# Kernel tuning notes

Measured on AMD Instinct MI355X. Metric: run time of the kernel, lower is better.

## Reference

```python
import jax, jax.numpy as jnp
import numpy as np

N_NODES = 50000
N_EDGES = 800000
N_REL = 16
N_GRAPHS = 64
IN_DIM = 128
HID = 128
FC = 256
N_CLASSES = 16


def setup_inputs() -> dict:
    key = jax.random.key(0)
    ks = jax.random.split(key, 16)
    h = jax.random.normal(ks[0], (N_NODES, IN_DIM), dtype=jnp.float32)
    src = jax.random.randint(ks[1], (N_EDGES,), 0, N_NODES, dtype=jnp.int32)
    dst = jax.random.randint(ks[2], (N_EDGES,), 0, N_NODES, dtype=jnp.int32)
    rel_types = jax.random.randint(ks[3], (N_EDGES,), 0, N_REL, dtype=jnp.int32)
    graph_ids = jnp.sort(jax.random.randint(ks[4], (N_NODES,), 0, N_GRAPHS, dtype=jnp.int32))
    s1 = 1.0 / np.sqrt(IN_DIM)
    s2 = 1.0 / np.sqrt(HID)
    # RGCN layer 1: per-relation weights, self-loop weight, bias
    W1 = jax.random.normal(ks[5], (N_REL, IN_DIM, HID), dtype=jnp.float32) * s1
    Ws1 = jax.random.normal(ks[6], (IN_DIM, HID), dtype=jnp.float32) * s1
    b1 = jnp.zeros((HID,), dtype=jnp.float32)
    # RGCN layer 2
    W2 = jax.random.normal(ks[7], (N_REL, HID, HID), dtype=jnp.float32) * s2
    Ws2 = jax.random.normal(ks[8], (HID, HID), dtype=jnp.float32) * s2
    b2 = jnp.zeros((HID,), dtype=jnp.float32)
    # FC layer after mean pooling
    Wfc = jax.random.normal(ks[9], (HID, FC), dtype=jnp.float32) * s2
    bfc = jnp.zeros((FC,), dtype=jnp.float32)
    # classify head
    Wc = jax.random.normal(ks[10], (FC, N_CLASSES), dtype=jnp.float32) * (1.0 / np.sqrt(FC))
    bc = jnp.zeros((N_CLASSES,), dtype=jnp.float32)
    return dict(h=h, src=src, dst=dst, rel_types=rel_types, graph_ids=graph_ids,
                W1=W1, Ws1=Ws1, b1=b1, W2=W2, Ws2=Ws2, b2=b2,
                Wfc=Wfc, bfc=bfc, Wc=Wc, bc=bc)


def _rel_graph_conv(h, W, Ws, b, src, dst, rel):
    # dgl RelGraphConv (regularizer=None, self_loop=True, bias=True):
    # out[v] = sum_{e:(u->v)} W[rel_e] @ h[u] + Ws @ h[v] + b
    hW = jnp.einsum('ni,rio->rno', h, W)            # [R, N, out]
    msg = hW[rel, src]                               # [E, out] gather per edge
    agg = jax.ops.segment_sum(msg, dst, num_segments=N_NODES)
    return agg + h @ Ws + b


def _mean_nodes(h, graph_ids):
    sums = jax.ops.segment_sum(h, graph_ids, num_segments=N_GRAPHS)      # [G, D]
    cnts = jax.ops.segment_sum(jnp.ones((h.shape[0], 1), h.dtype), graph_ids,
                               num_segments=N_GRAPHS)                    # [G, 1]
    return sums / jnp.maximum(cnts, 1.0)


def reference(h, src, dst, rel_types, graph_ids,
              W1, Ws1, b1, W2, Ws2, b2, Wfc, bfc, Wc, bc):
    h = h.astype(jnp.float32)
    h = jax.nn.relu(_rel_graph_conv(h, W1, Ws1, b1, src, dst, rel_types))
    h = jax.nn.relu(_rel_graph_conv(h, W2, Ws2, b2, src, dst, rel_types))
    hg = _mean_nodes(h, graph_ids)                   # [G, HID]
    hg = jax.nn.relu(hg @ Wfc + bfc)                 # [G, FC]
    return jax.nn.softmax(hg @ Wc + bc, axis=1)      # [G, n_classes]
```

## Files before the change

### kernel.cpp

```cpp
#include <hip/hip_runtime.h>
#include <hip/hip_bf16.h>

#define N_NODES   50000
#define N_PAD     50048
#define N_EDGES   800000
#define N_REL     16
#define N_GRAPHS  64
#define DIM       128
#define FC_DIM    256
#define N_CLASSES 16

#define NCOARSE   782
#define NCH       196
#define CHSZ      4096
#define POOL_CH   64

#define NBLK_CX   27200
#define XW_TOTAL  (N_PAD * DIM + 2 * 17 * 16384)

#define WS_HG     0
#define WS_CNT    32768
#define MEMSET_SZ 33024
#define WS_BLKH   33024
#define WS_COFS   646400
#define WS_RTMP   649728
#define WS_RECS   3849728
#define WS_OFFSDR 7049728
#define WS_X1     10253056
#define WS_X2     23065344
#define WS_AGG    35877632
#define WS_WB     48689920

typedef __attribute__((ext_vector_type(8))) short bf16x8;
typedef __attribute__((ext_vector_type(4))) float f32x4;

__device__ __forceinline__ void atomAddF(float* p, float v) {
#if defined(__gfx90a__) || defined(__gfx942__) || defined(__gfx950__)
    unsafeAtomicAdd(p, v);
#else
    atomicAdd(p, v);
#endif
}

__device__ __forceinline__ float bf2f(unsigned int u) {
    union { float f; unsigned int i; } x; x.i = u << 16; return x.f;
}
__device__ __forceinline__ unsigned short f2bf(float f) {
    union { float f; unsigned int u; } x; x.f = f;
    unsigned int r = x.u + 0x7fff + ((x.u >> 16) & 1);
    return (unsigned short)(r >> 16);
}
__device__ __forceinline__ void accum8(float* qa, uint4 u) {
    qa[0] += bf2f(u.x & 0xffff); qa[1] += bf2f(u.x >> 16);
    qa[2] += bf2f(u.y & 0xffff); qa[3] += bf2f(u.y >> 16);
    qa[4] += bf2f(u.z & 0xffff); qa[5] += bf2f(u.z >> 16);
    qa[6] += bf2f(u.w & 0xffff); qa[7] += bf2f(u.w >> 16);
}
__device__ __forceinline__ void pack16(const float* qa, unsigned short* dst) {
    #pragma unroll
    for (int j = 0; j < 2; ++j) {
        uint4 w;
        w.x = ((unsigned int)f2bf(qa[j*8+1]) << 16) | f2bf(qa[j*8+0]);
        w.y = ((unsigned int)f2bf(qa[j*8+3]) << 16) | f2bf(qa[j*8+2]);
        w.z = ((unsigned int)f2bf(qa[j*8+5]) << 16) | f2bf(qa[j*8+4]);
        w.w = ((unsigned int)f2bf(qa[j*8+7]) << 16) | f2bf(qa[j*8+6]);
        ((uint4*)dst)[j] = w;
    }
}

__global__ __launch_bounds__(256) void k_h1cx(
    const int* __restrict__ dst,
    int* __restrict__ blockHist,
    const float* __restrict__ h, unsigned short* __restrict__ x1,
    const float* __restrict__ W1, const float* __restrict__ Ws1,
    const float* __restrict__ W2, const float* __restrict__ Ws2,
    unsigned short* __restrict__ Wb)
{
    __shared__ int hl[NCOARSE];
    int t = threadIdx.x;
    if (blockIdx.x < NCH) {
        int b = blockIdx.x;
        for (int i = t; i < NCOARSE; i += 256) hl[i] = 0;
        __syncthreads();
        int e0 = b * CHSZ;
        int eend = min(e0 + CHSZ, N_EDGES);
        for (int e = e0 + t; e < eend; e += 256)
            atomicAdd(&hl[dst[e] >> 6], 1);
        __syncthreads();
        for (int i = t; i < NCOARSE; i += 256) blockHist[b * NCOARSE + i] = hl[i];
    } else {
        int id = (blockIdx.x - NCH) * 256 + t;
        if (id < N_PAD * DIM) {
            int v = id >> 7;
            x1[id] = (v < N_NODES) ? f2bf(h[id]) : (unsigned short)0;
        } else {
            int tt = id - N_PAD * DIM;
            int l = tt / 278528, rem = tt % 278528;
            int r = rem >> 14, rr = rem & 16383;
            int n = rr >> 7, k = rr & 127;
            const float* W  = l ? W2 : W1;
            const float* Ws = l ? Ws2 : Ws1;
            float v = (r < 16) ? W[r * 16384 + k * 128 + n] : Ws[k * 128 + n];
            Wb[tt] = f2bf(v);
        }
    }
}

__global__ __launch_bounds__(256) void k_csA(int* __restrict__ blockHist,
                                             int* __restrict__ cOffs)
{
    __shared__ int sc[2][256];
    int i = blockIdx.x, t = threadIdx.x;
    int v = (t < NCH) ? blockHist[t * NCOARSE + i] : 0;
    sc[0][t] = v; __syncthreads();
    int cur = 0;
    for (int o = 1; o < 256; o <<= 1) {
        sc[cur ^ 1][t] = sc[cur][t] + ((t >= o) ? sc[cur][t - o] : 0);
        __syncthreads();
        cur ^= 1;
    }
    if (t < NCH) blockHist[t * NCOARSE + i] = sc[cur][t] - v;
    if (t == NCH - 1) cOffs[i] = sc[cur][t];
}

__global__ __launch_bounds__(1024) void k_csB(int* __restrict__ cOffs)
{
    __shared__ int c1[1024], c2[1024];
    int t = threadIdx.x;
    int v = (t < NCOARSE) ? cOffs[t] : 0;
    c1[t] = v; __syncthreads();
    int* cur = c1; int* nxt = c2;
    for (int o = 1; o < 1024; o <<= 1) {
        nxt[t] = cur[t] + ((t >= o) ? cur[t - o] : 0);
        __syncthreads();
        int* tmp = cur; cur = nxt; nxt = tmp;
    }
    if (t < NCOARSE) cOffs[t] = cur[t] - v;
    if (t == NCOARSE) cOffs[NCOARSE] = cur[NCOARSE - 1];
}

__global__ __launch_bounds__(256) void k_scat1(
    const int* __restrict__ src, const int* __restrict__ dst, const int* __restrict__ rel,
    const int* __restrict__ blockHist, const int* __restrict__ cOffs,
    unsigned int* __restrict__ rtmp)
{
    __shared__ int baseL[NCOARSE];
    __shared__ int hl[NCOARSE];
    int b = blockIdx.x, t = threadIdx.x;
    for (int i = t; i < NCOARSE; i += 256) {
        baseL[i] = blockHist[b * NCOARSE + i] + cOffs[i];
        hl[i] = 0;
    }
    __syncthreads();
    int e0 = b * CHSZ;
    int eend = min(e0 + CHSZ, N_EDGES);
    for (int e = e0 + t; e < eend; e += 256) {
        int d = dst[e];
        int c = d >> 6;
        int rank = atomicAdd(&hl[c], 1);
        rtmp[baseL[c] + rank] = ((unsigned int)src[e] << 10)
                              | ((unsigned int)(d & 63) << 4)
                              | (unsigned int)rel[e];
    }
}

__global__ __launch_bounds__(256) void k_p2(
    const unsigned int* __restrict__ rtmp, const int* __restrict__ cOffs,
    unsigned int* __restrict__ recs, int* __restrict__ offsDR)
{
    __shared__ int cnt[1024];
    __shared__ int part[256], part2[256];
    int i = blockIdx.x, t = threadIdx.x;
    int segB = cOffs[i], segE = cOffs[i + 1];
    for (int k = t; k < 1024; k += 256) cnt[k] = 0;
    __syncthreads();
    for (int e = segB + t; e < segE; e += 256)
        atomicAdd(&cnt[rtmp[e] & 1023u], 1);
    __syncthreads();
    int b4 = t * 4;
    int s0 = cnt[b4], s1 = cnt[b4+1], s2 = cnt[b4+2], s3 = cnt[b4+3];
    int tsum = s0 + s1 + s2 + s3;
    part[t] = tsum;
    __syncthreads();
    int* cur = part; int* nxt = part2;
    for (int o = 1; o < 256; o <<= 1) {
        nxt[t] = cur[t] + ((t >= o) ? cur[t - o] : 0);
        __syncthreads();
        int* tmp = cur; cur = nxt; nxt = tmp;
    }
    int excl = cur[t] - tsum + segB;
    cnt[b4]     = excl;
    cnt[b4 + 1] = excl + s0;
    cnt[b4 + 2] = excl + s0 + s1;
    cnt[b4 + 3] = excl + s0 + s1 + s2;
    __syncthreads();
    for (int k = t; k < 1024; k += 256) offsDR[i * 1024 + k] = cnt[k];
    if (i == NCOARSE - 1 && t == 0) offsDR[NCOARSE * 1024] = segE;
    for (int e = segB + t; e < segE; e += 256) {
        unsigned int r = rtmp[e];
        int pos = atomicAdd(&cnt[r & 1023u], 1);
        recs[pos] = r >> 10;
    }
}

__global__ __launch_bounds__(256) void k_rgcn(
    const unsigned short* __restrict__ x, const unsigned short* __restrict__ Wb,
    const unsigned int* __restrict__ recs, const int* __restrict__ offsDR,
    const float* __restrict__ bias, unsigned short* __restrict__ out, int relu)
{
    __shared__ __attribute__((aligned(16))) unsigned short S[64 * 136];
    __shared__ int sOffs[1025];
    int tid = threadIdx.x;
    int bin = blockIdx.x;
    int v0 = bin * 64;
    for (int k = tid; k < 1025; k += 256) sOffs[k] = offsDR[bin * 1024 + k];

    int w = tid >> 6, l = tid & 63, nl = l & 15, q = l >> 4;
    int gh = tid >> 3, s = tid & 7;

    f32x4 acc[4][2];
    #pragma unroll
    for (int m = 0; m < 4; ++m) {
        acc[m][0] = (f32x4){0.f, 0.f, 0.f, 0.f};
        acc[m][1] = (f32x4){0.f, 0.f, 0.f, 0.f};
    }
    __syncthreads();

    for (int r = 0; r < 17; ++r) {
        #pragma unroll
        for (int hf = 0; hf < 2; ++hf) {
            int g = hf * 32 + gh;
            float qa[16];
            #pragma unroll
            for (int j = 0; j < 16; ++j) qa[j] = 0.f;
            if (r == 16) {
                const uint4* xp = (const uint4*)(x + (size_t)(v0 + g) * DIM + s * 16);
                uint4 u0 = xp[0], u1 = xp[1];
                accum8(qa, u0); accum8(qa + 8, u1);
            } else {
                int o0 = sOffs[g * 16 + r], o1 = sOffs[g * 16 + r + 1];
                for (int e = o0; e < o1; ++e) {
                    const uint4* xp = (const uint4*)(x + (size_t)recs[e] * DIM + s * 16);
                    uint4 u0 = xp[0], u1 = xp[1];
                    accum8(qa, u0); accum8(qa + 8, u1);
                }
            }
            pack16(qa, &S[g * 136 + s * 16]);
        }
        __syncthreads();
        const unsigned short* wr = Wb + r * 16384;
        #pragma unroll
        for (int kc = 0; kc < 4; ++kc) {
            bf16x8 b0 = *(const bf16x8*)(wr + (w * 32 + nl) * 128 + kc * 32 + q * 8);
            bf16x8 b1 = *(const bf16x8*)(wr + (w * 32 + 16 + nl) * 128 + kc * 32 + q * 8);
            #pragma unroll
            for (int m = 0; m < 4; ++m) {
                bf16x8 a = *(const bf16x8*)(&S[(m * 16 + nl) * 136 + kc * 32 + q * 8]);
                acc[m][0] = __builtin_amdgcn_mfma_f32_16x16x32_bf16(a, b0, acc[m][0], 0, 0, 0);
                acc[m][1] = __builtin_amdgcn_mfma_f32_16x16x32_bf16(a, b1, acc[m][1], 0, 0, 0);
            }
        }
        __syncthreads();
    }

    float bv0 = bias[w * 32 + nl], bv1 = bias[w * 32 + 16 + nl];
    #pragma unroll
    for (int m = 0; m < 4; ++m) {
        #pragma unroll
        for (int reg = 0; reg < 4; ++reg) {
            int row = m * 16 + q * 4 + reg;
            float f0 = acc[m][0][reg] + bv0;
            float f1 = acc[m][1][reg] + bv1;
            if (relu) { f0 = fmaxf(f0, 0.f); f1 = fmaxf(f1, 0.f); }
            S[row * 136 + (w * 32 + nl)]      = f2bf(f0);
            S[row * 136 + (w * 32 + 16 + nl)] = f2bf(f1);
        }
    }
    __syncthreads();
    {
        unsigned short* Ob = out + (size_t)v0 * DIM;
        #pragma unroll
        for (int it = 0; it < 4; ++it) {
            int c = tid + it * 256;
            int rw = c >> 4, k8 = c & 15;
            uint4 vv = *(const uint4*)(&S[rw * 136 + k8 * 8]);
            *(uint4*)(Ob + rw * DIM + k8 * 8) = vv;
        }
    }
}

__global__ void k_pool(const unsigned short* __restrict__ agg2, const int* __restrict__ gids,
                       float* __restrict__ hg_sum, int* __restrict__ cnt)
{
    int d  = threadIdx.x;
    int n0 = blockIdx.x * POOL_CH;
    int nend = min(n0 + POOL_CH, N_NODES);
    if (n0 >= N_NODES) return;
    int curg = gids[n0];
    float run = 0.f;
    for (int n = n0; n < nend; ++n) {
        int g = gids[n];
        if (g != curg) { atomAddF(&hg_sum[curg*DIM + d], run); run = 0.f; curg = g; }
        run += fmaxf(bf2f((unsigned int)agg2[n*DIM + d]), 0.f);
    }
    atomAddF(&hg_sum[curg*DIM + d], run);
    if (d == 0) {
        int cg = gids[n0]; int rl = 0;
        for (int n = n0; n < nend; ++n) {
            int g = gids[n];
            if (g != cg) { atomicAdd(&cnt[cg], rl); rl = 0; cg = g; }
            rl++;
        }
        atomicAdd(&cnt[cg], rl);
    }
}

__global__ __launch_bounds__(256) void k_head(
    const float* __restrict__ hg_sum, const int* __restrict__ cnt,
    const float* __restrict__ Wfc, const float* __restrict__ bfc,
    const float* __restrict__ Wc, const float* __restrict__ bc,
    float* __restrict__ out)
{
    int g = blockIdx.x, t = threadIdx.x;
    __shared__ float hgl[DIM];
    __shared__ float fcl[FC_DIM];
    __shared__ float lg[N_CLASSES];
    if (t < DIM) {
        float c = (float)max(cnt[g], 1);
        hgl[t] = hg_sum[g*DIM + t] / c;
    }
    __syncthreads();
    {
        float sv = bfc[t];
        #pragma unroll 4
        for (int k = 0; k < DIM; ++k) sv += hgl[k] * Wfc[k*FC_DIM + t];
        fcl[t] = fmaxf(sv, 0.f);
    }
    __syncthreads();
    if (t < N_CLASSES) {
        float lgt = bc[t];
        #pragma unroll 4
        for (int k = 0; k < FC_DIM; ++k) lgt += fcl[k] * Wc[k*N_CLASSES + t];
        lg[t] = lgt;
    }
    __syncthreads();
    if (t < N_CLASSES) {
        float m = lg[0];
        #pragma unroll
        for (int c = 1; c < N_CLASSES; ++c) m = fmaxf(m, lg[c]);
        float sden = 0.f;
        #pragma unroll
        for (int c = 0; c < N_CLASSES; ++c) sden += expf(lg[c] - m);
        out[g*N_CLASSES + t] = expf(lg[t] - m) / sden;
    }
}

extern "C" void kernel_launch(void* const* d_in, const int* in_sizes, int n_in,
                              void* d_out, int out_size, void* d_ws, size_t ws_size,
                              hipStream_t stream)
{
    const float* h   = (const float*)d_in[0];
    const int*   src = (const int*)d_in[1];
    const int*   dst = (const int*)d_in[2];
    const int*   rel = (const int*)d_in[3];
    const int*   gid = (const int*)d_in[4];
    const float* W1  = (const float*)d_in[5];
    const float* Ws1 = (const float*)d_in[6];
    const float* b1  = (const float*)d_in[7];
    const float* W2  = (const float*)d_in[8];
    const float* Ws2 = (const float*)d_in[9];
    const float* b2  = (const float*)d_in[10];
    const float* Wfc = (const float*)d_in[11];
    const float* bfc = (const float*)d_in[12];
    const float* Wc  = (const float*)d_in[13];
    const float* bc  = (const float*)d_in[14];
    float* out = (float*)d_out;

    char* ws = (char*)d_ws;
    float* hgsum = (float*)(ws + WS_HG);
    int*   cnt   = (int*)(ws + WS_CNT);
    int*   blkH  = (int*)(ws + WS_BLKH);
    int*   cOffs = (int*)(ws + WS_COFS);
    unsigned int* rtmp = (unsigned int*)(ws + WS_RTMP);
    unsigned int* recs = (unsigned int*)(ws + WS_RECS);
    int*   offsDR = (int*)(ws + WS_OFFSDR);
    unsigned short* x1  = (unsigned short*)(ws + WS_X1);
    unsigned short* x2  = (unsigned short*)(ws + WS_X2);
    unsigned short* agg = (unsigned short*)(ws + WS_AGG);
    unsigned short* Wb  = (unsigned short*)(ws + WS_WB);

    hipMemsetAsync(ws + WS_HG, 0, MEMSET_SZ, stream);

    k_h1cx<<<NCH + NBLK_CX, 256, 0, stream>>>(dst, blkH, h, x1, W1, Ws1, W2, Ws2, Wb);
    k_csA<<<NCOARSE, 256, 0, stream>>>(blkH, cOffs);
    k_csB<<<1, 1024, 0, stream>>>(cOffs);
    k_scat1<<<NCH, 256, 0, stream>>>(src, dst, rel, blkH, cOffs, rtmp);
    k_p2<<<NCOARSE, 256, 0, stream>>>(rtmp, cOffs, recs, offsDR);

    k_rgcn<<<NCOARSE, 256, 0, stream>>>(x1, Wb, recs, offsDR, b1, x2, 1);
    k_rgcn<<<NCOARSE, 256, 0, stream>>>(x2, Wb + 17 * 16384, recs, offsDR, b2, agg, 0);

    k_pool<<<(N_PAD + POOL_CH - 1) / POOL_CH, 128, 0, stream>>>(agg, gid, hgsum, cnt);
    k_head<<<N_GRAPHS, 256, 0, stream>>>(hgsum, cnt, Wfc, bfc, Wc, bc, out);
}
```

Before: 449.0 us.

## Halve RGCN node bins to 32 nodes and unroll edge gathers by four

Shrinks the coarse destination bin from 64 to 32 nodes, which doubles the number of RGCN blocks (1564) and halves each block's shared memory and accumulator registers. The scan, scatter and sort kernels are updated to match the new bin count and record encoding. The per-relation gather loop is unrolled by four so each thread has several independent row loads in flight. The cost is reloading the relation weights from memory in twice as many blocks, and each block issues half as many MFMAs per weight fetch.

```diff
diff --git a/kernel.cpp b/kernel.cpp
--- a/kernel.cpp
+++ b/kernel.cpp
@@ -10,7 +10,7 @@
 #define FC_DIM    256
 #define N_CLASSES 16
 
-#define NCOARSE   782
+#define NCOARSE   1564
 #define NCH       196
 #define CHSZ      4096
 #define POOL_CH   64
@@ -22,14 +22,14 @@
 #define WS_CNT    32768
 #define MEMSET_SZ 33024
 #define WS_BLKH   33024
-#define WS_COFS   646400
-#define WS_RTMP   649728
-#define WS_RECS   3849728
-#define WS_OFFSDR 7049728
-#define WS_X1     10253056
-#define WS_X2     23065344
-#define WS_AGG    35877632
-#define WS_WB     48689920
+#define WS_COFS   1259520
+#define WS_RTMP   1265920
+#define WS_RECS   4465920
+#define WS_OFFSDR 7665920
+#define WS_X1     10869248
+#define WS_X2     23681536
+#define WS_AGG    36493824
+#define WS_WB     49306112
 
 typedef __attribute__((ext_vector_type(8))) short bf16x8;
 typedef __attribute__((ext_vector_type(4))) float f32x4;
@@ -85,7 +85,7 @@
         int e0 = b * CHSZ;
         int eend = min(e0 + CHSZ, N_EDGES);
         for (int e = e0 + t; e < eend; e += 256)
-            atomicAdd(&hl[dst[e] >> 6], 1);
+            atomicAdd(&hl[dst[e] >> 5], 1);
         __syncthreads();
         for (int i = t; i < NCOARSE; i += 256) blockHist[b * NCOARSE + i] = hl[i];
     } else {
@@ -127,16 +127,21 @@
 {
     __shared__ int c1[1024], c2[1024];
     int t = threadIdx.x;
-    int v = (t < NCOARSE) ? cOffs[t] : 0;
-    c1[t] = v; __syncthreads();
+    int i0 = 2 * t, i1 = 2 * t + 1;
+    int v0 = (i0 < NCOARSE) ? cOffs[i0] : 0;
+    int v1 = (i1 < NCOARSE) ? cOffs[i1] : 0;
+    int p = v0 + v1;
+    c1[t] = p; __syncthreads();
     int* cur = c1; int* nxt = c2;
     for (int o = 1; o < 1024; o <<= 1) {
         nxt[t] = cur[t] + ((t >= o) ? cur[t - o] : 0);
         __syncthreads();
         int* tmp = cur; cur = nxt; nxt = tmp;
     }
-    if (t < NCOARSE) cOffs[t] = cur[t] - v;
-    if (t == NCOARSE) cOffs[NCOARSE] = cur[NCOARSE - 1];
+    int ex = cur[t] - p;
+    if (i0 < NCOARSE) cOffs[i0] = ex;
+    if (i1 < NCOARSE) cOffs[i1] = ex + v0;
+    if (t == 1023) cOffs[NCOARSE] = cur[1023];
 }
 
 __global__ __launch_bounds__(256) void k_scat1(
@@ -156,10 +161,10 @@
     int eend = min(e0 + CHSZ, N_EDGES);
     for (int e = e0 + t; e < eend; e += 256) {
         int d = dst[e];
-        int c = d >> 6;
+        int c = d >> 5;
         int rank = atomicAdd(&hl[c], 1);
-        rtmp[baseL[c] + rank] = ((unsigned int)src[e] << 10)
-                              | ((unsigned int)(d & 63) << 4)
+        rtmp[baseL[c] + rank] = ((unsigned int)src[e] << 9)
+                              | ((unsigned int)(d & 31) << 4)
                               | (unsigned int)rel[e];
     }
 }
@@ -168,18 +173,17 @@
     const unsigned int* __restrict__ rtmp, const int* __restrict__ cOffs,
     unsigned int* __restrict__ recs, int* __restrict__ offsDR)
 {
-    __shared__ int cnt[1024];
+    __shared__ int cnt[512];
     __shared__ int part[256], part2[256];
     int i = blockIdx.x, t = threadIdx.x;
     int segB = cOffs[i], segE = cOffs[i + 1];
-    for (int k = t; k < 1024; k += 256) cnt[k] = 0;
+    cnt[t] = 0; cnt[t + 256] = 0;
     __syncthreads();
     for (int e = segB + t; e < segE; e += 256)
-        atomicAdd(&cnt[rtmp[e] & 1023u], 1);
-    __syncthreads();
-    int b4 = t * 4;
-    int s0 = cnt[b4], s1 = cnt[b4+1], s2 = cnt[b4+2], s3 = cnt[b4+3];
-    int tsum = s0 + s1 + s2 + s3;
+        atomicAdd(&cnt[rtmp[e] & 511u], 1);
+    __syncthreads();
+    int s0 = cnt[2 * t], s1 = cnt[2 * t + 1];
+    int tsum = s0 + s1;
     part[t] = tsum;
     __syncthreads();
     int* cur = part; int* nxt = part2;
@@ -189,17 +193,16 @@
         int* tmp = cur; cur = nxt; nxt = tmp;
     }
     int excl = cur[t] - tsum + segB;
-    cnt[b4]     = excl;
-    cnt[b4 + 1] = excl + s0;
-    cnt[b4 + 2] = excl + s0 + s1;
-    cnt[b4 + 3] = excl + s0 + s1 + s2;
-    __syncthreads();
-    for (int k = t; k < 1024; k += 256) offsDR[i * 1024 + k] = cnt[k];
-    if (i == NCOARSE - 1 && t == 0) offsDR[NCOARSE * 1024] = segE;
+    cnt[2 * t]     = excl;
+    cnt[2 * t + 1] = excl + s0;
+    offsDR[i * 512 + 2 * t]     = excl;
+    offsDR[i * 512 + 2 * t + 1] = excl + s0;
+    if (i == NCOARSE - 1 && t == 0) offsDR[NCOARSE * 512] = segE;
+    __syncthreads();
     for (int e = segB + t; e < segE; e += 256) {
         unsigned int r = rtmp[e];
-        int pos = atomicAdd(&cnt[r & 1023u], 1);
-        recs[pos] = r >> 10;
+        int pos = atomicAdd(&cnt[r & 511u], 1);
+        recs[pos] = r >> 9;
     }
 }
 
@@ -208,45 +211,55 @@
     const unsigned int* __restrict__ recs, const int* __restrict__ offsDR,
     const float* __restrict__ bias, unsigned short* __restrict__ out, int relu)
 {
-    __shared__ __attribute__((aligned(16))) unsigned short S[64 * 136];
-    __shared__ int sOffs[1025];
+    __shared__ __attribute__((aligned(16))) unsigned short S[32 * 136];
+    __shared__ int sOffs[513];
     int tid = threadIdx.x;
     int bin = blockIdx.x;
-    int v0 = bin * 64;
-    for (int k = tid; k < 1025; k += 256) sOffs[k] = offsDR[bin * 1024 + k];
+    int v0 = bin * 32;
+    for (int k = tid; k < 513; k += 256) sOffs[k] = offsDR[bin * 512 + k];
 
     int w = tid >> 6, l = tid & 63, nl = l & 15, q = l >> 4;
-    int gh = tid >> 3, s = tid & 7;
-
-    f32x4 acc[4][2];
+    int g = tid >> 3, s = tid & 7;
+
+    f32x4 acc[2][2];
     #pragma unroll
-    for (int m = 0; m < 4; ++m) {
+    for (int m = 0; m < 2; ++m) {
         acc[m][0] = (f32x4){0.f, 0.f, 0.f, 0.f};
         acc[m][1] = (f32x4){0.f, 0.f, 0.f, 0.f};
     }
     __syncthreads();
 
     for (int r = 0; r < 17; ++r) {
-        #pragma unroll
-        for (int hf = 0; hf < 2; ++hf) {
-            int g = hf * 32 + gh;
-            float qa[16];
-            #pragma unroll
-            for (int j = 0; j < 16; ++j) qa[j] = 0.f;
-            if (r == 16) {
-                const uint4* xp = (const uint4*)(x + (size_t)(v0 + g) * DIM + s * 16);
+        float qa[16];
+        #pragma unroll
+        for (int j = 0; j < 16; ++j) qa[j] = 0.f;
+        if (r == 16) {
+            const uint4* xp = (const uint4*)(x + (size_t)(v0 + g) * DIM + s * 16);
+            uint4 u0 = xp[0], u1 = xp[1];
+            accum8(qa, u0); accum8(qa + 8, u1);
+        } else {
+            int o0 = sOffs[g * 16 + r], o1 = sOffs[g * 16 + r + 1];
+            int e = o0;
+            for (; e + 3 < o1; e += 4) {
+                unsigned int c0 = recs[e], c1 = recs[e+1], c2 = recs[e+2], c3 = recs[e+3];
+                const uint4* p0 = (const uint4*)(x + (size_t)c0 * DIM + s * 16);
+                const uint4* p1 = (const uint4*)(x + (size_t)c1 * DIM + s * 16);
+                const uint4* p2 = (const uint4*)(x + (size_t)c2 * DIM + s * 16);
+                const uint4* p3 = (const uint4*)(x + (size_t)c3 * DIM + s * 16);
+                uint4 a0 = p0[0], a1 = p0[1], b0 = p1[0], b1 = p1[1];
+                uint4 e0v = p2[0], e1v = p2[1], f0v = p3[0], f1v = p3[1];
+                accum8(qa, a0);  accum8(qa + 8, a1);
+                accum8(qa, b0);  accum8(qa + 8, b1);
+                accum8(qa, e0v); accum8(qa + 8, e1v);
+                accum8(qa, f0v); accum8(qa + 8, f1v);
+            }
+            for (; e < o1; ++e) {
+                const uint4* xp = (const uint4*)(x + (size_t)recs[e] * DIM + s * 16);
                 uint4 u0 = xp[0], u1 = xp[1];
                 accum8(qa, u0); accum8(qa + 8, u1);
-            } else {
-                int o0 = sOffs[g * 16 + r], o1 = sOffs[g * 16 + r + 1];
-                for (int e = o0; e < o1; ++e) {
-                    const uint4* xp = (const uint4*)(x + (size_t)recs[e] * DIM + s * 16);
-                    uint4 u0 = xp[0], u1 = xp[1];
-                    accum8(qa, u0); accum8(qa + 8, u1);
-                }
             }
-            pack16(qa, &S[g * 136 + s * 16]);
-        }
+        }
+        pack16(qa, &S[g * 136 + s * 16]);
         __syncthreads();
         const unsigned short* wr = Wb + r * 16384;
         #pragma unroll
@@ -254,7 +267,7 @@
             bf16x8 b0 = *(const bf16x8*)(wr + (w * 32 + nl) * 128 + kc * 32 + q * 8);
             bf16x8 b1 = *(const bf16x8*)(wr + (w * 32 + 16 + nl) * 128 + kc * 32 + q * 8);
             #pragma unroll
-            for (int m = 0; m < 4; ++m) {
+            for (int m = 0; m < 2; ++m) {
                 bf16x8 a = *(const bf16x8*)(&S[(m * 16 + nl) * 136 + kc * 32 + q * 8]);
                 acc[m][0] = __builtin_amdgcn_mfma_f32_16x16x32_bf16(a, b0, acc[m][0], 0, 0, 0);
                 acc[m][1] = __builtin_amdgcn_mfma_f32_16x16x32_bf16(a, b1, acc[m][1], 0, 0, 0);
@@ -265,7 +278,7 @@
 
     float bv0 = bias[w * 32 + nl], bv1 = bias[w * 32 + 16 + nl];
     #pragma unroll
-    for (int m = 0; m < 4; ++m) {
+    for (int m = 0; m < 2; ++m) {
         #pragma unroll
         for (int reg = 0; reg < 4; ++reg) {
             int row = m * 16 + q * 4 + reg;
@@ -280,7 +293,7 @@
     {
         unsigned short* Ob = out + (size_t)v0 * DIM;
         #pragma unroll
-        for (int it = 0; it < 4; ++it) {
+        for (int it = 0; it < 2; ++it) {
             int c = tid + it * 256;
             int rw = c >> 4, k8 = c & 15;
             uint4 vv = *(const uint4*)(&S[rw * 136 + k8 * 8]);
```

Result: slower. 536.4 us (+19.5%).

## Sort edges relation-major per bin and gather via shared-memory float atomics

Applied to the files above, without the earlier changes.

Records within each 64-node bin are now sorted relation-major instead of destination-major, so each relation's edges form one contiguous range. All 32 edge groups then process those edges in parallel, accumulating into a shared fp32 tile with LDS atomics. The next relation's gather overlaps with the current relation's MFMA, and the self-loop term loads the node rows directly. This removes the load imbalance of one thread group walking a single destination's edges, at the cost of many LDS atomic adds and a larger shared-memory footprint (about 34KB for accL) that may lower occupancy.

```diff
diff --git a/kernel.cpp b/kernel.cpp
--- a/kernel.cpp
+++ b/kernel.cpp
@@ -56,16 +56,11 @@
     qa[4] += bf2f(u.z & 0xffff); qa[5] += bf2f(u.z >> 16);
     qa[6] += bf2f(u.w & 0xffff); qa[7] += bf2f(u.w >> 16);
 }
-__device__ __forceinline__ void pack16(const float* qa, unsigned short* dst) {
-    #pragma unroll
-    for (int j = 0; j < 2; ++j) {
-        uint4 w;
-        w.x = ((unsigned int)f2bf(qa[j*8+1]) << 16) | f2bf(qa[j*8+0]);
-        w.y = ((unsigned int)f2bf(qa[j*8+3]) << 16) | f2bf(qa[j*8+2]);
-        w.z = ((unsigned int)f2bf(qa[j*8+5]) << 16) | f2bf(qa[j*8+4]);
-        w.w = ((unsigned int)f2bf(qa[j*8+7]) << 16) | f2bf(qa[j*8+6]);
-        ((uint4*)dst)[j] = w;
-    }
+__device__ __forceinline__ void atomAcc8(float* ar, uint4 u) {
+    atomicAdd(&ar[0], bf2f(u.x & 0xffff)); atomicAdd(&ar[1], bf2f(u.x >> 16));
+    atomicAdd(&ar[2], bf2f(u.y & 0xffff)); atomicAdd(&ar[3], bf2f(u.y >> 16));
+    atomicAdd(&ar[4], bf2f(u.z & 0xffff)); atomicAdd(&ar[5], bf2f(u.z >> 16));
+    atomicAdd(&ar[6], bf2f(u.w & 0xffff)); atomicAdd(&ar[7], bf2f(u.w >> 16));
 }
 
 __global__ __launch_bounds__(256) void k_h1cx(
@@ -159,8 +154,8 @@
         int c = d >> 6;
         int rank = atomicAdd(&hl[c], 1);
         rtmp[baseL[c] + rank] = ((unsigned int)src[e] << 10)
-                              | ((unsigned int)(d & 63) << 4)
-                              | (unsigned int)rel[e];
+                              | ((unsigned int)rel[e] << 6)
+                              | (unsigned int)(d & 63);
     }
 }
 
@@ -189,17 +184,20 @@
         int* tmp = cur; cur = nxt; nxt = tmp;
     }
     int excl = cur[t] - tsum + segB;
+    offsDR[i * 1024 + b4]     = excl;
+    offsDR[i * 1024 + b4 + 1] = excl + s0;
+    offsDR[i * 1024 + b4 + 2] = excl + s0 + s1;
+    offsDR[i * 1024 + b4 + 3] = excl + s0 + s1 + s2;
+    if (i == NCOARSE - 1 && t == 0) offsDR[NCOARSE * 1024] = segE;
     cnt[b4]     = excl;
     cnt[b4 + 1] = excl + s0;
     cnt[b4 + 2] = excl + s0 + s1;
     cnt[b4 + 3] = excl + s0 + s1 + s2;
     __syncthreads();
-    for (int k = t; k < 1024; k += 256) offsDR[i * 1024 + k] = cnt[k];
-    if (i == NCOARSE - 1 && t == 0) offsDR[NCOARSE * 1024] = segE;
     for (int e = segB + t; e < segE; e += 256) {
         unsigned int r = rtmp[e];
         int pos = atomicAdd(&cnt[r & 1023u], 1);
-        recs[pos] = r >> 10;
+        recs[pos] = ((r >> 10) << 6) | (r & 63u);
     }
 }
 
@@ -208,60 +206,108 @@
     const unsigned int* __restrict__ recs, const int* __restrict__ offsDR,
     const float* __restrict__ bias, unsigned short* __restrict__ out, int relu)
 {
+    __shared__ float accL[64][133];
     __shared__ __attribute__((aligned(16))) unsigned short S[64 * 136];
-    __shared__ int sOffs[1025];
+    __shared__ int sOffs[17];
     int tid = threadIdx.x;
     int bin = blockIdx.x;
     int v0 = bin * 64;
-    for (int k = tid; k < 1025; k += 256) sOffs[k] = offsDR[bin * 1024 + k];
+    if (tid < 17) sOffs[tid] = offsDR[bin * 1024 + tid * 64];
+    {
+        float* af = &accL[0][0];
+        for (int k = tid; k < 64 * 133; k += 256) af[k] = 0.f;
+    }
+    __syncthreads();
 
     int w = tid >> 6, l = tid & 63, nl = l & 15, q = l >> 4;
-    int gh = tid >> 3, s = tid & 7;
-
-    f32x4 acc[4][2];
+    int es = tid & 7, eg = tid >> 3;
+
+    f32x4 racc[4][2];
     #pragma unroll
     for (int m = 0; m < 4; ++m) {
-        acc[m][0] = (f32x4){0.f, 0.f, 0.f, 0.f};
-        acc[m][1] = (f32x4){0.f, 0.f, 0.f, 0.f};
-    }
-    __syncthreads();
-
-    for (int r = 0; r < 17; ++r) {
-        #pragma unroll
-        for (int hf = 0; hf < 2; ++hf) {
-            int g = hf * 32 + gh;
-            float qa[16];
+        racc[m][0] = (f32x4){0.f, 0.f, 0.f, 0.f};
+        racc[m][1] = (f32x4){0.f, 0.f, 0.f, 0.f};
+    }
+
+    auto edgepass = [&](int rr) {
+        int o0 = sOffs[rr], o1 = sOffs[rr + 1];
+        for (int e = o0 + eg; e < o1; e += 32) {
+            unsigned int rec = recs[e];
+            int dl = rec & 63;
+            const uint4* xp = (const uint4*)(x + ((size_t)(rec >> 6)) * DIM + es * 16);
+            uint4 u0 = xp[0], u1 = xp[1];
+            float* ar = &accL[dl][es * 16];
+            atomAcc8(ar, u0);
+            atomAcc8(ar + 8, u1);
+        }
+    };
+
+    edgepass(0);
+    __syncthreads();
+
+    for (int r = 0; r < 16; ++r) {
+        {
+            int crow = tid >> 2, cc = tid & 3;
+            float* ap = &accL[crow][cc * 32];
+            unsigned int* sp = (unsigned int*)&S[crow * 136 + cc * 32];
             #pragma unroll
-            for (int j = 0; j < 16; ++j) qa[j] = 0.f;
-            if (r == 16) {
-                const uint4* xp = (const uint4*)(x + (size_t)(v0 + g) * DIM + s * 16);
-                uint4 u0 = xp[0], u1 = xp[1];
-                accum8(qa, u0); accum8(qa + 8, u1);
-            } else {
-                int o0 = sOffs[g * 16 + r], o1 = sOffs[g * 16 + r + 1];
-                for (int e = o0; e < o1; ++e) {
-                    const uint4* xp = (const uint4*)(x + (size_t)recs[e] * DIM + s * 16);
-                    uint4 u0 = xp[0], u1 = xp[1];
-                    accum8(qa, u0); accum8(qa + 8, u1);
+            for (int j = 0; j < 16; ++j) {
+                float f0 = ap[2*j], f1 = ap[2*j + 1];
+                sp[j] = ((unsigned int)f2bf(f1) << 16) | f2bf(f0);
+                ap[2*j] = 0.f; ap[2*j + 1] = 0.f;
+            }
+        }
+        __syncthreads();
+        {
+            const unsigned short* wr = Wb + r * 16384;
+            bf16x8 b0[4], b1[4];
+            #pragma unroll
+            for (int kc = 0; kc < 4; ++kc) {
+                b0[kc] = *(const bf16x8*)(wr + (w * 32 + nl) * 128 + kc * 32 + q * 8);
+                b1[kc] = *(const bf16x8*)(wr + (w * 32 + 16 + nl) * 128 + kc * 32 + q * 8);
+            }
+            #pragma unroll
+            for (int kc = 0; kc < 4; ++kc) {
+                #pragma unroll
+                for (int m = 0; m < 4; ++m) {
+                    bf16x8 a = *(const bf16x8*)(&S[(m * 16 + nl) * 136 + kc * 32 + q * 8]);
+                    racc[m][0] = __builtin_amdgcn_mfma_f32_16x16x32_bf16(a, b0[kc], racc[m][0], 0, 0, 0);
+                    racc[m][1] = __builtin_amdgcn_mfma_f32_16x16x32_bf16(a, b1[kc], racc[m][1], 0, 0, 0);
                 }
             }
-            pack16(qa, &S[g * 136 + s * 16]);
-        }
-        __syncthreads();
-        const unsigned short* wr = Wb + r * 16384;
+        }
+        if (r < 15) edgepass(r + 1);
+        __syncthreads();
+    }
+
+    #pragma unroll
+    for (int hf = 0; hf < 2; ++hf) {
+        int g = hf * 32 + eg;
+        const uint4* xp = (const uint4*)(x + (size_t)(v0 + g) * DIM + es * 16);
+        uint4 u0 = xp[0], u1 = xp[1];
+        *(uint4*)(&S[g * 136 + es * 16])     = u0;
+        *(uint4*)(&S[g * 136 + es * 16 + 8]) = u1;
+    }
+    __syncthreads();
+    {
+        const unsigned short* wr = Wb + 16 * 16384;
+        bf16x8 b0[4], b1[4];
         #pragma unroll
         for (int kc = 0; kc < 4; ++kc) {
-            bf16x8 b0 = *(const bf16x8*)(wr + (w * 32 + nl) * 128 + kc * 32 + q * 8);
-            bf16x8 b1 = *(const bf16x8*)(wr + (w * 32 + 16 + nl) * 128 + kc * 32 + q * 8);
+            b0[kc] = *(const bf16x8*)(wr + (w * 32 + nl) * 128 + kc * 32 + q * 8);
+            b1[kc] = *(const bf16x8*)(wr + (w * 32 + 16 + nl) * 128 + kc * 32 + q * 8);
+        }
+        #pragma unroll
+        for (int kc = 0; kc < 4; ++kc) {
             #pragma unroll
             for (int m = 0; m < 4; ++m) {
                 bf16x8 a = *(const bf16x8*)(&S[(m * 16 + nl) * 136 + kc * 32 + q * 8]);
-                acc[m][0] = __builtin_amdgcn_mfma_f32_16x16x32_bf16(a, b0, acc[m][0], 0, 0, 0);
-                acc[m][1] = __builtin_amdgcn_mfma_f32_16x16x32_bf16(a, b1, acc[m][1], 0, 0, 0);
+                racc[m][0] = __builtin_amdgcn_mfma_f32_16x16x32_bf16(a, b0[kc], racc[m][0], 0, 0, 0);
+                racc[m][1] = __builtin_amdgcn_mfma_f32_16x16x32_bf16(a, b1[kc], racc[m][1], 0, 0, 0);
             }
         }
-        __syncthreads();
-    }
+    }
+    __syncthreads();
 
     float bv0 = bias[w * 32 + nl], bv1 = bias[w * 32 + 16 + nl];
     #pragma unroll
@@ -269,8 +315,8 @@
         #pragma unroll
         for (int reg = 0; reg < 4; ++reg) {
             int row = m * 16 + q * 4 + reg;
-            float f0 = acc[m][0][reg] + bv0;
-            float f1 = acc[m][1][reg] + bv1;
+            float f0 = racc[m][0][reg] + bv0;
+            float f1 = racc[m][1][reg] + bv1;
             if (relu) { f0 = fmaxf(f0, 0.f); f1 = fmaxf(f1, 0.f); }
             S[row * 136 + (w * 32 + nl)]      = f2bf(f0);
             S[row * 136 + (w * 32 + 16 + nl)] = f2bf(f1);
```

Result: slower. 1.738 ms (+287.2%).
